# Performance work log

Hardware: AMD Instinct MI355X
Metric: run time of the kernel (lower is better)

## Reference

```python
import jax, jax.numpy as jnp
import numpy as np

N_QUBITS = 16
N_LAYERS = 2
NUM_CLASSES = 10
BATCH = 256

# CNOT as (c_out, t_out, c_in, t_in)
_CNOT = np.zeros((2, 2, 2, 2), dtype=np.complex64)
_CNOT[0, 0, 0, 0] = 1; _CNOT[0, 1, 0, 1] = 1
_CNOT[1, 1, 1, 0] = 1; _CNOT[1, 0, 1, 1] = 1
CNOT = jnp.asarray(_CNOT)


def rot_matrix(phi, theta, omega):
    # PennyLane Rot = RZ(omega) @ RY(theta) @ RZ(phi)
    c, s = jnp.cos(theta / 2), jnp.sin(theta / 2)
    m00 = jnp.exp(-0.5j * (phi + omega)) * c
    m01 = -jnp.exp(0.5j * (phi - omega)) * s
    m10 = jnp.exp(-0.5j * (phi - omega)) * s
    m11 = jnp.exp(0.5j * (phi + omega)) * c
    return jnp.stack([jnp.stack([m00, m01]), jnp.stack([m10, m11])]).astype(jnp.complex64)


def apply_1q(state, U, w, n):
    # state: (B, 2**n); wire 0 = most-significant bit (PennyLane convention)
    B = state.shape[0]
    st = state.reshape(B, 2 ** w, 2, -1)
    st = jnp.einsum('oi,baic->baoc', U, st)
    return st.reshape(B, -1)


def apply_cnot(state, c, t, n):
    B = state.shape[0]
    st = state.reshape((B,) + (2,) * n)
    st = jnp.tensordot(CNOT, st, axes=[[2, 3], [c + 1, t + 1]])  # new c,t axes at front
    st = jnp.moveaxis(st, [0, 1], [c + 1, t + 1])
    return st.reshape(B, -1)


def circuit_expvals(x, q_params, n, n_layers):
    # AmplitudeEmbedding with normalize=True
    norm = jnp.sqrt(jnp.sum(x * x, axis=-1, keepdims=True))
    psi = (x / norm).astype(jnp.complex64)
    for l in range(n_layers):
        for w in range(n):
            U = rot_matrix(q_params[l, w, 0], q_params[l, w, 1], q_params[l, w, 2])
            psi = apply_1q(psi, U, w, n)
        r = (l % (n - 1)) + 1  # default StronglyEntanglingLayers ranges
        for w in range(n):
            psi = apply_cnot(psi, w, (w + r) % n, n)
    probs = psi.real ** 2 + psi.imag ** 2  # (B, 2**n)
    B = probs.shape[0]
    ev = []
    for w in range(n):
        p = probs.reshape(B, 2 ** w, 2, -1)
        ev.append(p[:, :, 0, :].sum(axis=(1, 2)) - p[:, :, 1, :].sum(axis=(1, 2)))
    return jnp.stack(ev, axis=1)  # (B, n)


def setup_inputs() -> dict:
    key = jax.random.key(0)
    k1, k2, k3, k4 = jax.random.split(key, 4)
    x = jax.random.normal(k1, (BATCH, 2 ** N_QUBITS), dtype=jnp.float32)
    q_params = jax.random.normal(k2, (N_LAYERS, N_QUBITS, 3), dtype=jnp.float32)
    lim = 1.0 / np.sqrt(N_QUBITS)
    W = jax.random.uniform(k3, (NUM_CLASSES, N_QUBITS), jnp.float32, -lim, lim)
    b = jax.random.uniform(k4, (NUM_CLASSES,), jnp.float32, -lim, lim)
    return {"x": x, "q_params": q_params, "W": W, "b": b}


def reference(x, q_params, W, b):
    feats = circuit_expvals(x, q_params, N_QUBITS, N_LAYERS)  # (B, n_qubits)
    return feats @ W.T + b
```

## Files before the change

kernel.cpp:

```cpp
#include <hip/hip_runtime.h>


#define BATCH 256
#define NCLS 10

typedef float v2f __attribute__((ext_vector_type(2)));
typedef _Float16 f16x2 __attribute__((ext_vector_type(2)));

struct CircuitMeta { unsigned l1mask[16]; unsigned l1role[16]; unsigned fin[16]; };

__host__ __device__ constexpr CircuitMeta make_meta() {
  CircuitMeta m{};
  unsigned col[16], inv[16];
  for (int w = 0; w < 16; ++w) { col[w] = 1u << (15 - w); inv[w] = 1u << (15 - w); }
  for (int w = 0; w < 16; ++w) { int c = w, t = (w + 1) & 15; col[c] ^= col[t]; inv[t] ^= inv[c]; }
  for (int w = 0; w < 16; ++w) { m.l1mask[w] = col[w]; m.l1role[w] = inv[w]; }
  for (int w = 0; w < 16; ++w) { int c = w, t = (w + 2) & 15; col[c] ^= col[t]; inv[t] ^= inv[c]; }
  for (int w = 0; w < 16; ++w) m.fin[w] = inv[w];
  return m;
}
constexpr CircuitMeta META = make_meta();

__host__ __device__ constexpr unsigned HASH(unsigned i) {
  return i ^ ((i >> 4) & 15u) ^ ((i >> 8) & 15u);
}

__device__ __forceinline__ v2f swp(v2f a) { return __builtin_shufflevector(a, a, 1, 0); }

__device__ __forceinline__ unsigned PK(v2f a) {
  return __builtin_bit_cast(unsigned, __builtin_amdgcn_cvt_pkrtz(a.x, a.y));
}
__device__ __forceinline__ v2f UNPK(unsigned u) {
  f16x2 h = __builtin_bit_cast(f16x2, u);
  return (v2f){(float)h.x, (float)h.y};
}

template<int B0,int B1,int B2,int B3,int B4>
__host__ __device__ constexpr unsigned regval5(int j) {
  return ((unsigned)(j & 1) << B0) | ((unsigned)((j >> 1) & 1) << B1) |
         ((unsigned)((j >> 2) & 1) << B2) | ((unsigned)((j >> 3) & 1) << B3) |
         ((unsigned)((j >> 4) & 1) << B4);
}

template<int B0,int B1,int B2,int B3,int B4, unsigned MG, unsigned RG>
__device__ __forceinline__ void gate5(v2f (&A)[32], const float* __restrict__ g,
                                      int gi, unsigned tp) {
  constexpr unsigned cover = (1u<<B0)|(1u<<B1)|(1u<<B2)|(1u<<B3)|(1u<<B4);
  static_assert((MG & ~cover) == 0u, "gate mask not covered by stage reg bits");
  constexpr unsigned mr = ((MG>>B0)&1u) | (((MG>>B1)&1u)<<1) | (((MG>>B2)&1u)<<2)
                        | (((MG>>B3)&1u)<<3) | (((MG>>B4)&1u)<<4);
  static_assert(mr != 0u, "empty reg mask");
  constexpr unsigned pivot = mr & (0u - mr);

  float u00r = g[gi*8+0], u00i = g[gi*8+1], u01r = g[gi*8+2], u01i = g[gi*8+3];
  float u10r = g[gi*8+4], u10i = g[gi*8+5], u11r = g[gi*8+6], u11i = g[gi*8+7];
  const bool s = (__popc(RG & tp) & 1) != 0;
  float e00r = s ? u11r : u00r, e00i = s ? u11i : u00i;
  float e01r = s ? u10r : u01r, e01i = s ? u10i : u01i;
  float e10r = s ? u01r : u10r, e10i = s ? u01i : u10i;
  float e11r = s ? u00r : u11r, e11i = s ? u00i : u11i;
  v2f a00 = {e00r, e00r}, b00 = {-e00i, e00i};
  v2f a01 = {e01r, e01r}, b01 = {-e01i, e01i};
  v2f a10 = {e10r, e10r}, b10 = {-e10i, e10i};
  v2f a11 = {e11r, e11r}, b11 = {-e11i, e11i};

  #pragma unroll
  for (int j0 = 0; j0 < 32; ++j0) {
    if (j0 & (int)pivot) continue;
    const int j1 = j0 ^ (int)mr;
    const bool podd =
      (__builtin_popcount(RG & regval5<B0,B1,B2,B3,B4>(j0)) & 1) != 0;
    v2f v0 = A[j0], v1 = A[j1];
    v2f v0s = swp(v0), v1s = swp(v1);
    if (!podd) {
      A[j0] = a00*v0 + b00*v0s + a01*v1 + b01*v1s;
      A[j1] = a10*v0 + b10*v0s + a11*v1 + b11*v1s;
    } else {
      A[j0] = a11*v0 + b11*v0s + a10*v1 + b10*v1s;
      A[j1] = a01*v0 + b01*v0s + a00*v1 + b00*v1s;
    }
  }
}

__global__ void prep_gates(const float* __restrict__ qp, float* __restrict__ g) {
  int i = threadIdx.x;
  if (i >= 32) return;
  float phi = qp[i*3+0], th = qp[i*3+1], om = qp[i*3+2];
  float cth = cosf(0.5f*th), sth = sinf(0.5f*th);
  float a = 0.5f*(phi+om), d = 0.5f*(phi-om);
  float ca = cosf(a), sa = sinf(a), cd = cosf(d), sd = sinf(d);
  g[i*8+0] =  ca*cth; g[i*8+1] = -sa*cth;
  g[i*8+2] = -cd*sth; g[i*8+3] = -sd*sth;
  g[i*8+4] =  cd*sth; g[i*8+5] = -sd*sth;
  g[i*8+6] =  ca*cth; g[i*8+7] =  sa*cth;
}

__global__ __launch_bounds__(256, 4) void passA(const float* __restrict__ x,
    unsigned* __restrict__ st, const float* __restrict__ g) {
  __shared__ unsigned L[8192];
  const int t = threadIdx.x;
  const int batch = blockIdx.x >> 3;
  const unsigned f = blockIdx.x & 7;
  const float* xb = x + ((size_t)batch << 16) + ((size_t)f << 13);

  v2f A[32];
  #pragma unroll
  for (int j = 0; j < 32; ++j) A[j] = (v2f){xb[((unsigned)j << 8) | (unsigned)t], 0.f};

  gate5<8,9,10,11,12, 0x1000u,0x1000u>(A, g, 3, 0u);
  gate5<8,9,10,11,12, 0x0800u,0x0800u>(A, g, 4, 0u);
  gate5<8,9,10,11,12, 0x0400u,0x0400u>(A, g, 5, 0u);
  gate5<8,9,10,11,12, 0x0200u,0x0200u>(A, g, 6, 0u);
  gate5<8,9,10,11,12, 0x0100u,0x0100u>(A, g, 7, 0u);

  {
    const unsigned wb = HASH((unsigned)t);
    #pragma unroll
    for (int j = 0; j < 32; ++j) L[wb ^ HASH((unsigned)j << 8)] = PK(A[j]);
    __syncthreads();
    const unsigned rb = HASH((((unsigned)t & 0xF8u) << 5) | ((unsigned)t & 7u));
    #pragma unroll
    for (int j = 0; j < 32; ++j) A[j] = UNPK(L[rb ^ HASH((unsigned)j << 3)]);
  }

  gate5<3,4,5,6,7, 0x0080u,0x0080u>(A, g,  8, 0u);
  gate5<3,4,5,6,7, 0x0040u,0x0040u>(A, g,  9, 0u);
  gate5<3,4,5,6,7, 0x0020u,0x0020u>(A, g, 10, 0u);
  gate5<3,4,5,6,7, 0x0010u,0x0010u>(A, g, 11, 0u);
  gate5<3,4,5,6,7, 0x0008u,0x0008u>(A, g, 12, 0u);

  __syncthreads();
  {
    const unsigned wb = HASH((((unsigned)t & 0xF8u) << 5) | ((unsigned)t & 7u));
    #pragma unroll
    for (int j = 0; j < 32; ++j) L[wb ^ HASH((unsigned)j << 3)] = PK(A[j]);
    __syncthreads();
    const unsigned rb = HASH((unsigned)t << 3);
    #pragma unroll
    for (int j = 0; j < 32; ++j)
      A[j] = UNPK(L[rb ^ HASH(((unsigned)j & 7u) | (((unsigned)j & 24u) << 8))]);
  }

  gate5<0,1,2,11,12, 0x0004u,0x0004u>(A, g, 13, 0u);
  gate5<0,1,2,11,12, 0x0002u,0x0002u>(A, g, 14, 0u);
  gate5<0,1,2,11,12, 0x0001u,0x0001u>(A, g, 15, 0u);

  unsigned* outb = st + ((size_t)batch << 16) + ((size_t)f << 13);
  #pragma unroll
  for (int jh = 0; jh < 4; ++jh) {
    uint4 q0, q1;
    q0.x = PK(A[jh*8+0]); q0.y = PK(A[jh*8+1]); q0.z = PK(A[jh*8+2]); q0.w = PK(A[jh*8+3]);
    q1.x = PK(A[jh*8+4]); q1.y = PK(A[jh*8+5]); q1.z = PK(A[jh*8+6]); q1.w = PK(A[jh*8+7]);
    const unsigned si = ((unsigned)jh << 11) | ((unsigned)t << 3);
    *(uint4*)(outb + si) = q0;
    *(uint4*)(outb + si + 4) = q1;
  }
}

__global__ __launch_bounds__(256, 4) void passB(unsigned* __restrict__ st,
    const float* __restrict__ g) {
  __shared__ unsigned L[8192];
  const int t = threadIdx.x;
  const int batch = blockIdx.x >> 3;
  const unsigned c = blockIdx.x & 7;
  unsigned* stb = st + ((size_t)batch << 16);

  const unsigned lbase = ((unsigned)t & 127u) | (((unsigned)t & 128u) << 3) | (c << 7);
  v2f A[32];
  #pragma unroll
  for (int j = 0; j < 32; ++j) A[j] = UNPK(stb[((unsigned)j << 11) | lbase]);

  const unsigned tp1 = lbase;
  gate5<11,12,13,14,15, 0x8000u,0x8000u>(A, g, 0, tp1);
  gate5<11,12,13,14,15, 0x4000u,0x4000u>(A, g, 1, tp1);
  gate5<11,12,13,14,15, 0x2000u,0x2000u>(A, g, 2, tp1);
  gate5<11,12,13,14,15, META.l1mask[0], META.l1role[0]>(A, g, 16, tp1);
  gate5<11,12,13,14,15, META.l1mask[1], META.l1role[1]>(A, g, 17, tp1);
  gate5<11,12,13,14,15, META.l1mask[2], META.l1role[2]>(A, g, 18, tp1);
  gate5<11,12,13,14,15, META.l1mask[3], META.l1role[3]>(A, g, 19, tp1);

  {
    const unsigned wb = HASH((unsigned)t);
    #pragma unroll
    for (int j = 0; j < 32; ++j) L[wb ^ HASH((unsigned)j << 8)] = PK(A[j]);
    __syncthreads();
    const unsigned rb = HASH((((unsigned)t & 0xF0u) << 5) | (((unsigned)t & 15u) << 1));
    #pragma unroll
    for (int j = 0; j < 32; ++j)
      A[j] = UNPK(L[rb ^ HASH(((unsigned)j & 1u) | (((unsigned)j & 30u) << 4))]);
  }

  const unsigned tp2 = (((unsigned)t & 0xF0u) << 8) | (((unsigned)t & 15u) << 1) | (c << 7);
  gate5<0,5,6,10,11, META.l1mask[4], META.l1role[4]>(A, g, 20, tp2);
  gate5<0,5,6,10,11, META.l1mask[9], META.l1role[9]>(A, g, 25, tp2);

  __syncthreads();
  {
    const unsigned wb = HASH((((unsigned)t & 0xF0u) << 5) | (((unsigned)t & 15u) << 1));
    #pragma unroll
    for (int j = 0; j < 32; ++j)
      L[wb ^ HASH(((unsigned)j & 1u) | (((unsigned)j & 30u) << 4))] = PK(A[j]);
    __syncthreads();
    const unsigned rb = HASH((((unsigned)t & 0xFEu) << 5) | ((unsigned)t & 1u));
    #pragma unroll
    for (int j = 0; j < 32; ++j) A[j] = UNPK(L[rb ^ HASH((unsigned)j << 1)]);
  }

  const unsigned tp3 = (((unsigned)t & 0xFCu) << 8) | (((unsigned)t & 2u) << 5)
                     | ((unsigned)t & 1u) | (c << 7);
  gate5<1,2,3,4,5, META.l1mask[10], META.l1role[10]>(A, g, 26, tp3);
  gate5<1,2,3,4,5, META.l1mask[11], META.l1role[11]>(A, g, 27, tp3);
  gate5<1,2,3,4,5, META.l1mask[12], META.l1role[12]>(A, g, 28, tp3);
  gate5<1,2,3,4,5, META.l1mask[13], META.l1role[13]>(A, g, 29, tp3);

  __syncthreads();
  {
    const unsigned wb = HASH((((unsigned)t & 0xFEu) << 5) | ((unsigned)t & 1u));
    #pragma unroll
    for (int j = 0; j < 32; ++j) L[wb ^ HASH((unsigned)j << 1)] = PK(A[j]);
    __syncthreads();
    const unsigned rb = HASH((unsigned)t << 2);
    #pragma unroll
    for (int j = 0; j < 32; ++j)
      A[j] = UNPK(L[rb ^ HASH(((unsigned)j & 3u) | (((unsigned)j & 28u) << 8))]);
  }

  const unsigned tp4 = (((unsigned)t & 0xE0u) << 5) | (((unsigned)t & 31u) << 2) | (c << 7);
  gate5<0,1,13,14,15, META.l1mask[14], META.l1role[14]>(A, g, 30, tp4);
  gate5<0,1,13,14,15, META.l1mask[15], META.l1role[15]>(A, g, 31, tp4);

  #pragma unroll
  for (int jh = 0; jh < 8; ++jh) {
    uint4 q;
    q.x = PK(A[jh*4+0]); q.y = PK(A[jh*4+1]); q.z = PK(A[jh*4+2]); q.w = PK(A[jh*4+3]);
    *(uint4*)(stb + (tp4 | ((unsigned)jh << 13))) = q;
  }
}

__global__ __launch_bounds__(256, 4) void passC(const unsigned* __restrict__ st,
    const float* __restrict__ g, float* __restrict__ partials) {
  __shared__ float R[4][17];
  const int t = threadIdx.x;
  const int batch = blockIdx.x >> 3;
  const unsigned f = blockIdx.x & 7;
  const unsigned* stb = st + ((size_t)batch << 16);

  const unsigned cbase = (f << 13) | (((unsigned)t & 192u) << 5) | ((unsigned)t & 63u);
  v2f A[32];
  #pragma unroll
  for (int j = 0; j < 32; ++j) A[j] = UNPK(stb[cbase | ((unsigned)j << 6)]);

  gate5<6,7,8,9,10, META.l1mask[5], META.l1role[5]>(A, g, 21, cbase);
  gate5<6,7,8,9,10, META.l1mask[6], META.l1role[6]>(A, g, 22, cbase);
  gate5<6,7,8,9,10, META.l1mask[7], META.l1role[7]>(A, g, 23, cbase);
  gate5<6,7,8,9,10, META.l1mask[8], META.l1role[8]>(A, g, 24, cbase);

  float sv[16], tot = 0.f;
  #pragma unroll
  for (int w = 0; w < 16; ++w) sv[w] = 0.f;
  #pragma unroll
  for (int j = 0; j < 32; ++j) {
    const float pr = A[j].x*A[j].x + A[j].y*A[j].y;
    tot += pr;
    #pragma unroll
    for (int w = 0; w < 16; ++w) {
      const bool neg = (__builtin_popcount(META.fin[w] & ((unsigned)j << 6)) & 1) != 0;
      sv[w] += neg ? -pr : pr;
    }
  }
  #pragma unroll
  for (int w = 0; w < 16; ++w)
    if (__popc(META.fin[w] & cbase) & 1) sv[w] = -sv[w];

  #pragma unroll
  for (int off = 32; off; off >>= 1) {
    tot += __shfl_xor(tot, off, 64);
    #pragma unroll
    for (int w = 0; w < 16; ++w) sv[w] += __shfl_xor(sv[w], off, 64);
  }
  const int wave = t >> 6, lane = t & 63;
  if (lane == 0) {
    #pragma unroll
    for (int w = 0; w < 16; ++w) R[wave][w] = sv[w];
    R[wave][16] = tot;
  }
  __syncthreads();
  if (t < 17) {
    const float s2 = R[0][t] + R[1][t] + R[2][t] + R[3][t];
    partials[(size_t)blockIdx.x * 17 + t] = s2;
  }
}

__global__ __launch_bounds__(64) void head(const float* __restrict__ partials,
    const float* __restrict__ W, const float* __restrict__ bias,
    float* __restrict__ out) {
  const int b = blockIdx.x, tid = threadIdx.x;
  __shared__ float red[17];
  __shared__ float ev[16];
  if (tid < 17) {
    float s = 0.f;
    #pragma unroll
    for (int ch = 0; ch < 8; ++ch) s += partials[(size_t)((b << 3) + ch) * 17 + tid];
    red[tid] = s;
  }
  __syncthreads();
  if (tid < 16) ev[tid] = red[tid] / red[16];
  __syncthreads();
  if (tid < NCLS) {
    float o = bias[tid];
    #pragma unroll
    for (int w = 0; w < 16; ++w) o += ev[w] * W[tid*16 + w];
    out[b*NCLS + tid] = o;
  }
}

extern "C" void kernel_launch(void* const* d_in, const int* in_sizes, int n_in,
                              void* d_out, int out_size, void* d_ws, size_t ws_size,
                              hipStream_t stream) {
  const float* x  = (const float*)d_in[0];
  const float* qp = (const float*)d_in[1];
  const float* W  = (const float*)d_in[2];
  const float* bv = (const float*)d_in[3];
  float* out = (float*)d_out;

  unsigned* st     = (unsigned*)d_ws;
  float*    gates  = (float*)((char*)d_ws + (size_t)BATCH * 65536 * 4);
  float*    parts  = (float*)((char*)gates + 1024);

  prep_gates<<<dim3(1), dim3(64), 0, stream>>>(qp, gates);
  passA<<<dim3(BATCH*8), dim3(256), 0, stream>>>(x, st, gates);
  passB<<<dim3(BATCH*8), dim3(256), 0, stream>>>(st, gates);
  passC<<<dim3(BATCH*8), dim3(256), 0, stream>>>(st, gates, parts);
  head<<<dim3(BATCH), dim3(64), 0, stream>>>(parts, W, bv, out);
}
```

Baseline: 197.8 us.

## Fuse all passes into one per-batch kernel holding full state in LDS/registers

Replaces the three global-memory passes and the head kernel with a single kernel that runs one block of 1024 threads per batch element. Each thread holds 64 packed fp16 amplitudes in registers, and qubit reorderings are done through 128KB of dynamic LDS in two halves. Gates are regrouped into six stages, and the final reduction and linear head are folded into the same kernel. This removes the global state round-trips between passes and two kernel launches. In exchange it raises register pressure, allows only 256 blocks in the grid, and adds several barriers per exchange.

```diff
diff --git a/kernel.cpp b/kernel.cpp
--- a/kernel.cpp
+++ b/kernel.cpp
@@ -11,7 +11,7 @@
 
 __host__ __device__ constexpr CircuitMeta make_meta() {
   CircuitMeta m{};
-  unsigned col[16], inv[16];
+  unsigned col[16] = {}, inv[16] = {};
   for (int w = 0; w < 16; ++w) { col[w] = 1u << (15 - w); inv[w] = 1u << (15 - w); }
   for (int w = 0; w < 16; ++w) { int c = w, t = (w + 1) & 15; col[c] ^= col[t]; inv[t] ^= inv[c]; }
   for (int w = 0; w < 16; ++w) { m.l1mask[w] = col[w]; m.l1role[w] = inv[w]; }
@@ -21,12 +21,33 @@
 }
 constexpr CircuitMeta META = make_meta();
 
-__host__ __device__ constexpr unsigned HASH(unsigned i) {
-  return i ^ ((i >> 4) & 15u) ^ ((i >> 8) & 15u);
-}
+__host__ __device__ constexpr unsigned XH(unsigned q) {
+  return q ^ ((q >> 5) & 31u) ^ ((q >> 10) & 31u);
+}
+template<int H> __host__ __device__ constexpr unsigned QDROP(unsigned i) {
+  return (i & ((1u << H) - 1u)) | ((i >> (H + 1)) << H);
+}
+
+__host__ __device__ constexpr unsigned tg1(unsigned t){ return t << 2; }
+__host__ __device__ constexpr unsigned tg2(unsigned t){ return (t & 63u) | (((t >> 6) & 15u) << 12); }
+__host__ __device__ constexpr unsigned tg3(unsigned t){ return ((t & 31u) << 6) | (((t >> 5) & 15u) << 12) | (((t >> 9) & 1u) << 11); }
+__host__ __device__ constexpr unsigned tg4(unsigned t){ return (t & 31u) | (((t >> 5) & 15u) << 6) | (((t >> 9) & 1u) << 5); }
+__host__ __device__ constexpr unsigned tg5(unsigned t){ return (t & 31u) | (((t >> 5) & 31u) << 11); }
+__host__ __device__ constexpr unsigned tg6(unsigned t){ return ((t & 63u) << 4) | (((t >> 6) & 7u) << 11) | (((t >> 9) & 1u) << 10); }
+
+template<int B0,int B1,int B2,int B3,int B4,int B5>
+__host__ __device__ constexpr unsigned rv6b(unsigned j) {
+  return ((j & 1u) << B0) | (((j >> 1) & 1u) << B1) | (((j >> 2) & 1u) << B2) |
+         (((j >> 3) & 1u) << B3) | (((j >> 4) & 1u) << B4) | (((j >> 5) & 1u) << B5);
+}
+__host__ __device__ constexpr unsigned rv_s1(unsigned j){ return rv6b<0,1,12,13,14,15>(j); }
+__host__ __device__ constexpr unsigned rv_s2(unsigned j){ return rv6b<6,7,8,9,10,11>(j); }
+__host__ __device__ constexpr unsigned rv_s3(unsigned j){ return rv6b<0,1,2,3,4,5>(j); }
+__host__ __device__ constexpr unsigned rv_s4(unsigned j){ return rv6b<11,12,13,14,15,10>(j); }
+__host__ __device__ constexpr unsigned rv_s5(unsigned j){ return rv6b<5,6,7,8,9,10>(j); }
+__host__ __device__ constexpr unsigned rv_s6(unsigned j){ return rv6b<0,1,2,3,14,15>(j); }
 
 __device__ __forceinline__ v2f swp(v2f a) { return __builtin_shufflevector(a, a, 1, 0); }
-
 __device__ __forceinline__ unsigned PK(v2f a) {
   return __builtin_bit_cast(unsigned, __builtin_amdgcn_cvt_pkrtz(a.x, a.y));
 }
@@ -35,20 +56,13 @@
   return (v2f){(float)h.x, (float)h.y};
 }
 
-template<int B0,int B1,int B2,int B3,int B4>
-__host__ __device__ constexpr unsigned regval5(int j) {
-  return ((unsigned)(j & 1) << B0) | ((unsigned)((j >> 1) & 1) << B1) |
-         ((unsigned)((j >> 2) & 1) << B2) | ((unsigned)((j >> 3) & 1) << B3) |
-         ((unsigned)((j >> 4) & 1) << B4);
-}
-
-template<int B0,int B1,int B2,int B3,int B4, unsigned MG, unsigned RG>
-__device__ __forceinline__ void gate5(v2f (&A)[32], const float* __restrict__ g,
+template<int B0,int B1,int B2,int B3,int B4,int B5, unsigned MG, unsigned RG>
+__device__ __forceinline__ void gate6(unsigned (&A)[64], const float* __restrict__ g,
                                       int gi, unsigned tp) {
-  constexpr unsigned cover = (1u<<B0)|(1u<<B1)|(1u<<B2)|(1u<<B3)|(1u<<B4);
+  constexpr unsigned cover = (1u<<B0)|(1u<<B1)|(1u<<B2)|(1u<<B3)|(1u<<B4)|(1u<<B5);
   static_assert((MG & ~cover) == 0u, "gate mask not covered by stage reg bits");
   constexpr unsigned mr = ((MG>>B0)&1u) | (((MG>>B1)&1u)<<1) | (((MG>>B2)&1u)<<2)
-                        | (((MG>>B3)&1u)<<3) | (((MG>>B4)&1u)<<4);
+                        | (((MG>>B3)&1u)<<3) | (((MG>>B4)&1u)<<4) | (((MG>>B5)&1u)<<5);
   static_assert(mr != 0u, "empty reg mask");
   constexpr unsigned pivot = mr & (0u - mr);
 
@@ -65,19 +79,19 @@
   v2f a11 = {e11r, e11r}, b11 = {-e11i, e11i};
 
   #pragma unroll
-  for (int j0 = 0; j0 < 32; ++j0) {
+  for (int j0 = 0; j0 < 64; ++j0) {
     if (j0 & (int)pivot) continue;
     const int j1 = j0 ^ (int)mr;
     const bool podd =
-      (__builtin_popcount(RG & regval5<B0,B1,B2,B3,B4>(j0)) & 1) != 0;
-    v2f v0 = A[j0], v1 = A[j1];
+      (__builtin_popcount(RG & rv6b<B0,B1,B2,B3,B4,B5>((unsigned)j0)) & 1) != 0;
+    v2f v0 = UNPK(A[j0]), v1 = UNPK(A[j1]);
     v2f v0s = swp(v0), v1s = swp(v1);
     if (!podd) {
-      A[j0] = a00*v0 + b00*v0s + a01*v1 + b01*v1s;
-      A[j1] = a10*v0 + b10*v0s + a11*v1 + b11*v1s;
+      A[j0] = PK(a00*v0 + b00*v0s + a01*v1 + b01*v1s);
+      A[j1] = PK(a10*v0 + b10*v0s + a11*v1 + b11*v1s);
     } else {
-      A[j0] = a11*v0 + b11*v0s + a10*v1 + b10*v1s;
-      A[j1] = a01*v0 + b01*v0s + a00*v1 + b00*v1s;
+      A[j0] = PK(a11*v0 + b11*v0s + a10*v1 + b10*v1s);
+      A[j1] = PK(a01*v0 + b01*v0s + a00*v1 + b00*v1s);
     }
   }
 }
@@ -95,182 +109,143 @@
   g[i*8+6] =  ca*cth; g[i*8+7] =  sa*cth;
 }
 
-__global__ __launch_bounds__(256, 4) void passA(const float* __restrict__ x,
-    unsigned* __restrict__ st, const float* __restrict__ g) {
-  __shared__ unsigned L[8192];
-  const int t = threadIdx.x;
-  const int batch = blockIdx.x >> 3;
-  const unsigned f = blockIdx.x & 7;
-  const float* xb = x + ((size_t)batch << 16) + ((size_t)f << 13);
-
-  v2f A[32];
-  #pragma unroll
-  for (int j = 0; j < 32; ++j) A[j] = (v2f){xb[((unsigned)j << 8) | (unsigned)t], 0.f};
-
-  gate5<8,9,10,11,12, 0x1000u,0x1000u>(A, g, 3, 0u);
-  gate5<8,9,10,11,12, 0x0800u,0x0800u>(A, g, 4, 0u);
-  gate5<8,9,10,11,12, 0x0400u,0x0400u>(A, g, 5, 0u);
-  gate5<8,9,10,11,12, 0x0200u,0x0200u>(A, g, 6, 0u);
-  gate5<8,9,10,11,12, 0x0100u,0x0100u>(A, g, 7, 0u);
-
-  {
-    const unsigned wb = HASH((unsigned)t);
-    #pragma unroll
-    for (int j = 0; j < 32; ++j) L[wb ^ HASH((unsigned)j << 8)] = PK(A[j]);
-    __syncthreads();
-    const unsigned rb = HASH((((unsigned)t & 0xF8u) << 5) | ((unsigned)t & 7u));
-    #pragma unroll
-    for (int j = 0; j < 32; ++j) A[j] = UNPK(L[rb ^ HASH((unsigned)j << 3)]);
-  }
-
-  gate5<3,4,5,6,7, 0x0080u,0x0080u>(A, g,  8, 0u);
-  gate5<3,4,5,6,7, 0x0040u,0x0040u>(A, g,  9, 0u);
-  gate5<3,4,5,6,7, 0x0020u,0x0020u>(A, g, 10, 0u);
-  gate5<3,4,5,6,7, 0x0010u,0x0010u>(A, g, 11, 0u);
-  gate5<3,4,5,6,7, 0x0008u,0x0008u>(A, g, 12, 0u);
-
-  __syncthreads();
-  {
-    const unsigned wb = HASH((((unsigned)t & 0xF8u) << 5) | ((unsigned)t & 7u));
-    #pragma unroll
-    for (int j = 0; j < 32; ++j) L[wb ^ HASH((unsigned)j << 3)] = PK(A[j]);
-    __syncthreads();
-    const unsigned rb = HASH((unsigned)t << 3);
-    #pragma unroll
-    for (int j = 0; j < 32; ++j)
-      A[j] = UNPK(L[rb ^ HASH(((unsigned)j & 7u) | (((unsigned)j & 24u) << 8))]);
-  }
-
-  gate5<0,1,2,11,12, 0x0004u,0x0004u>(A, g, 13, 0u);
-  gate5<0,1,2,11,12, 0x0002u,0x0002u>(A, g, 14, 0u);
-  gate5<0,1,2,11,12, 0x0001u,0x0001u>(A, g, 15, 0u);
-
-  unsigned* outb = st + ((size_t)batch << 16) + ((size_t)f << 13);
-  #pragma unroll
-  for (int jh = 0; jh < 4; ++jh) {
-    uint4 q0, q1;
-    q0.x = PK(A[jh*8+0]); q0.y = PK(A[jh*8+1]); q0.z = PK(A[jh*8+2]); q0.w = PK(A[jh*8+3]);
-    q1.x = PK(A[jh*8+4]); q1.y = PK(A[jh*8+5]); q1.z = PK(A[jh*8+6]); q1.w = PK(A[jh*8+7]);
-    const unsigned si = ((unsigned)jh << 11) | ((unsigned)t << 3);
-    *(uint4*)(outb + si) = q0;
-    *(uint4*)(outb + si + 4) = q1;
-  }
-}
-
-__global__ __launch_bounds__(256, 4) void passB(unsigned* __restrict__ st,
-    const float* __restrict__ g) {
-  __shared__ unsigned L[8192];
-  const int t = threadIdx.x;
-  const int batch = blockIdx.x >> 3;
-  const unsigned c = blockIdx.x & 7;
-  unsigned* stb = st + ((size_t)batch << 16);
-
-  const unsigned lbase = ((unsigned)t & 127u) | (((unsigned)t & 128u) << 3) | (c << 7);
-  v2f A[32];
-  #pragma unroll
-  for (int j = 0; j < 32; ++j) A[j] = UNPK(stb[((unsigned)j << 11) | lbase]);
-
-  const unsigned tp1 = lbase;
-  gate5<11,12,13,14,15, 0x8000u,0x8000u>(A, g, 0, tp1);
-  gate5<11,12,13,14,15, 0x4000u,0x4000u>(A, g, 1, tp1);
-  gate5<11,12,13,14,15, 0x2000u,0x2000u>(A, g, 2, tp1);
-  gate5<11,12,13,14,15, META.l1mask[0], META.l1role[0]>(A, g, 16, tp1);
-  gate5<11,12,13,14,15, META.l1mask[1], META.l1role[1]>(A, g, 17, tp1);
-  gate5<11,12,13,14,15, META.l1mask[2], META.l1role[2]>(A, g, 18, tp1);
-  gate5<11,12,13,14,15, META.l1mask[3], META.l1role[3]>(A, g, 19, tp1);
-
-  {
-    const unsigned wb = HASH((unsigned)t);
-    #pragma unroll
-    for (int j = 0; j < 32; ++j) L[wb ^ HASH((unsigned)j << 8)] = PK(A[j]);
-    __syncthreads();
-    const unsigned rb = HASH((((unsigned)t & 0xF0u) << 5) | (((unsigned)t & 15u) << 1));
-    #pragma unroll
-    for (int j = 0; j < 32; ++j)
-      A[j] = UNPK(L[rb ^ HASH(((unsigned)j & 1u) | (((unsigned)j & 30u) << 4))]);
-  }
-
-  const unsigned tp2 = (((unsigned)t & 0xF0u) << 8) | (((unsigned)t & 15u) << 1) | (c << 7);
-  gate5<0,5,6,10,11, META.l1mask[4], META.l1role[4]>(A, g, 20, tp2);
-  gate5<0,5,6,10,11, META.l1mask[9], META.l1role[9]>(A, g, 25, tp2);
-
-  __syncthreads();
-  {
-    const unsigned wb = HASH((((unsigned)t & 0xF0u) << 5) | (((unsigned)t & 15u) << 1));
-    #pragma unroll
-    for (int j = 0; j < 32; ++j)
-      L[wb ^ HASH(((unsigned)j & 1u) | (((unsigned)j & 30u) << 4))] = PK(A[j]);
-    __syncthreads();
-    const unsigned rb = HASH((((unsigned)t & 0xFEu) << 5) | ((unsigned)t & 1u));
-    #pragma unroll
-    for (int j = 0; j < 32; ++j) A[j] = UNPK(L[rb ^ HASH((unsigned)j << 1)]);
-  }
-
-  const unsigned tp3 = (((unsigned)t & 0xFCu) << 8) | (((unsigned)t & 2u) << 5)
-                     | ((unsigned)t & 1u) | (c << 7);
-  gate5<1,2,3,4,5, META.l1mask[10], META.l1role[10]>(A, g, 26, tp3);
-  gate5<1,2,3,4,5, META.l1mask[11], META.l1role[11]>(A, g, 27, tp3);
-  gate5<1,2,3,4,5, META.l1mask[12], META.l1role[12]>(A, g, 28, tp3);
-  gate5<1,2,3,4,5, META.l1mask[13], META.l1role[13]>(A, g, 29, tp3);
-
-  __syncthreads();
-  {
-    const unsigned wb = HASH((((unsigned)t & 0xFEu) << 5) | ((unsigned)t & 1u));
-    #pragma unroll
-    for (int j = 0; j < 32; ++j) L[wb ^ HASH((unsigned)j << 1)] = PK(A[j]);
-    __syncthreads();
-    const unsigned rb = HASH((unsigned)t << 2);
-    #pragma unroll
-    for (int j = 0; j < 32; ++j)
-      A[j] = UNPK(L[rb ^ HASH(((unsigned)j & 3u) | (((unsigned)j & 28u) << 8))]);
-  }
-
-  const unsigned tp4 = (((unsigned)t & 0xE0u) << 5) | (((unsigned)t & 31u) << 2) | (c << 7);
-  gate5<0,1,13,14,15, META.l1mask[14], META.l1role[14]>(A, g, 30, tp4);
-  gate5<0,1,13,14,15, META.l1mask[15], META.l1role[15]>(A, g, 31, tp4);
-
-  #pragma unroll
-  for (int jh = 0; jh < 8; ++jh) {
-    uint4 q;
-    q.x = PK(A[jh*4+0]); q.y = PK(A[jh*4+1]); q.z = PK(A[jh*4+2]); q.w = PK(A[jh*4+3]);
-    *(uint4*)(stb + (tp4 | ((unsigned)jh << 13))) = q;
-  }
-}
-
-__global__ __launch_bounds__(256, 4) void passC(const unsigned* __restrict__ st,
-    const float* __restrict__ g, float* __restrict__ partials) {
-  __shared__ float R[4][17];
-  const int t = threadIdx.x;
-  const int batch = blockIdx.x >> 3;
-  const unsigned f = blockIdx.x & 7;
-  const unsigned* stb = st + ((size_t)batch << 16);
-
-  const unsigned cbase = (f << 13) | (((unsigned)t & 192u) << 5) | ((unsigned)t & 63u);
-  v2f A[32];
-  #pragma unroll
-  for (int j = 0; j < 32; ++j) A[j] = UNPK(stb[cbase | ((unsigned)j << 6)]);
-
-  gate5<6,7,8,9,10, META.l1mask[5], META.l1role[5]>(A, g, 21, cbase);
-  gate5<6,7,8,9,10, META.l1mask[6], META.l1role[6]>(A, g, 22, cbase);
-  gate5<6,7,8,9,10, META.l1mask[7], META.l1role[7]>(A, g, 23, cbase);
-  gate5<6,7,8,9,10, META.l1mask[8], META.l1role[8]>(A, g, 24, cbase);
+#define EXCH_TMP(HH, TGIN, RVIN, TGOUT, RVOUT)                                   \
+  {                                                                              \
+    const unsigned qbw = XH(QDROP<HH>(TGIN(t)));                                 \
+    const unsigned qbr = XH(QDROP<HH>(TGOUT(t)));                                \
+    const bool rlow = ((t >> 9) & 1u) == 0u;                                     \
+    _Pragma("unroll")                                                            \
+    for (int j = 0; j < 32; ++j) L[qbw ^ XH(QDROP<HH>(RVIN((unsigned)j)))] = A[j]; \
+    __syncthreads();                                                             \
+    if (rlow) {                                                                  \
+      _Pragma("unroll")                                                          \
+      for (int j = 0; j < 32; ++j) A[j] = L[qbr ^ XH(QDROP<HH>(RVOUT((unsigned)j)))]; \
+      _Pragma("unroll")                                                          \
+      for (int j = 0; j < 32; ++j) T[j] = L[qbr ^ XH(QDROP<HH>(RVOUT((unsigned)j + 32u)))]; \
+    }                                                                            \
+    __syncthreads();                                                             \
+    _Pragma("unroll")                                                            \
+    for (int j = 32; j < 64; ++j) L[qbw ^ XH(QDROP<HH>(RVIN((unsigned)j)))] = A[j]; \
+    __syncthreads();                                                             \
+    if (!rlow) {                                                                 \
+      _Pragma("unroll")                                                          \
+      for (int j = 0; j < 64; ++j) A[j] = L[qbr ^ XH(QDROP<HH>(RVOUT((unsigned)j)))]; \
+    } else {                                                                     \
+      _Pragma("unroll")                                                          \
+      for (int j = 0; j < 32; ++j) A[32 + j] = T[j];                             \
+    }                                                                            \
+    __syncthreads();                                                             \
+  }
+
+#define EXCH_SHR(HH, TGIN, RVIN, TGOUT, RVOUT)                                   \
+  {                                                                              \
+    const unsigned qbw = XH(QDROP<HH>(TGIN(t)));                                 \
+    const unsigned qbr = XH(QDROP<HH>(TGOUT(t)));                                \
+    _Pragma("unroll")                                                            \
+    for (int j = 0; j < 32; ++j) L[qbw ^ XH(QDROP<HH>(RVIN((unsigned)j)))] = A[j]; \
+    __syncthreads();                                                             \
+    _Pragma("unroll")                                                            \
+    for (int j = 0; j < 32; ++j) A[j] = L[qbr ^ XH(QDROP<HH>(RVOUT((unsigned)j)))]; \
+    __syncthreads();                                                             \
+    _Pragma("unroll")                                                            \
+    for (int j = 32; j < 64; ++j) L[qbw ^ XH(QDROP<HH>(RVIN((unsigned)j)))] = A[j]; \
+    __syncthreads();                                                             \
+    _Pragma("unroll")                                                            \
+    for (int j = 32; j < 64; ++j) A[j] = L[qbr ^ XH(QDROP<HH>(RVOUT((unsigned)j)))]; \
+    __syncthreads();                                                             \
+  }
+
+__global__ __launch_bounds__(1024, 4) void qsim(
+    const float* __restrict__ x, const float* __restrict__ g,
+    const float* __restrict__ W, const float* __restrict__ bias,
+    float* __restrict__ out)
+{
+  extern __shared__ unsigned L[];
+  const unsigned t = threadIdx.x;
+  unsigned A[64];
+  unsigned T[32];
+
+  const float4* xb = (const float4*)(x + ((size_t)blockIdx.x << 16));
+  #pragma unroll
+  for (int jh = 0; jh < 16; ++jh) {
+    float4 v = xb[((unsigned)jh << 10) | t];
+    A[jh*4+0] = PK((v2f){v.x, 0.f});
+    A[jh*4+1] = PK((v2f){v.y, 0.f});
+    A[jh*4+2] = PK((v2f){v.z, 0.f});
+    A[jh*4+3] = PK((v2f){v.w, 0.f});
+  }
+
+  const unsigned tp1 = tg1(t);
+  gate6<0,1,12,13,14,15, 0x8000u,0x8000u>(A, g,  0, tp1);
+  gate6<0,1,12,13,14,15, 0x4000u,0x4000u>(A, g,  1, tp1);
+  gate6<0,1,12,13,14,15, 0x2000u,0x2000u>(A, g,  2, tp1);
+  gate6<0,1,12,13,14,15, 0x1000u,0x1000u>(A, g,  3, tp1);
+  gate6<0,1,12,13,14,15, 0x0002u,0x0002u>(A, g, 14, tp1);
+  gate6<0,1,12,13,14,15, 0x0001u,0x0001u>(A, g, 15, tp1);
+
+  EXCH_TMP(15, tg1, rv_s1, tg2, rv_s2)
+
+  const unsigned tp2 = tg2(t);
+  gate6<6,7,8,9,10,11, 0x0800u,0x0800u>(A, g, 4, tp2);
+  gate6<6,7,8,9,10,11, 0x0400u,0x0400u>(A, g, 5, tp2);
+  gate6<6,7,8,9,10,11, 0x0200u,0x0200u>(A, g, 6, tp2);
+  gate6<6,7,8,9,10,11, 0x0100u,0x0100u>(A, g, 7, tp2);
+  gate6<6,7,8,9,10,11, 0x0080u,0x0080u>(A, g, 8, tp2);
+  gate6<6,7,8,9,10,11, 0x0040u,0x0040u>(A, g, 9, tp2);
+
+  EXCH_TMP(11, tg2, rv_s2, tg3, rv_s3)
+
+  const unsigned tp3 = tg3(t);
+  gate6<0,1,2,3,4,5, 0x0020u,0x0020u>(A, g, 10, tp3);
+  gate6<0,1,2,3,4,5, 0x0010u,0x0010u>(A, g, 11, tp3);
+  gate6<0,1,2,3,4,5, 0x0008u,0x0008u>(A, g, 12, tp3);
+  gate6<0,1,2,3,4,5, 0x0004u,0x0004u>(A, g, 13, tp3);
+  gate6<0,1,2,3,4,5, META.l1mask[10], META.l1role[10]>(A, g, 26, tp3);
+  gate6<0,1,2,3,4,5, META.l1mask[11], META.l1role[11]>(A, g, 27, tp3);
+  gate6<0,1,2,3,4,5, META.l1mask[12], META.l1role[12]>(A, g, 28, tp3);
+  gate6<0,1,2,3,4,5, META.l1mask[13], META.l1role[13]>(A, g, 29, tp3);
+  gate6<0,1,2,3,4,5, META.l1mask[14], META.l1role[14]>(A, g, 30, tp3);
+
+  EXCH_TMP(5, tg3, rv_s3, tg4, rv_s4)
+
+  const unsigned tp4 = tg4(t);
+  gate6<11,12,13,14,15,10, META.l1mask[0], META.l1role[0]>(A, g, 16, tp4);
+  gate6<11,12,13,14,15,10, META.l1mask[1], META.l1role[1]>(A, g, 17, tp4);
+  gate6<11,12,13,14,15,10, META.l1mask[2], META.l1role[2]>(A, g, 18, tp4);
+  gate6<11,12,13,14,15,10, META.l1mask[3], META.l1role[3]>(A, g, 19, tp4);
+  gate6<11,12,13,14,15,10, META.l1mask[4], META.l1role[4]>(A, g, 20, tp4);
+
+  EXCH_SHR(10, tg4, rv_s4, tg5, rv_s5)
+
+  const unsigned tp5 = tg5(t);
+  gate6<5,6,7,8,9,10, META.l1mask[5], META.l1role[5]>(A, g, 21, tp5);
+  gate6<5,6,7,8,9,10, META.l1mask[6], META.l1role[6]>(A, g, 22, tp5);
+  gate6<5,6,7,8,9,10, META.l1mask[7], META.l1role[7]>(A, g, 23, tp5);
+  gate6<5,6,7,8,9,10, META.l1mask[8], META.l1role[8]>(A, g, 24, tp5);
+  gate6<5,6,7,8,9,10, META.l1mask[9], META.l1role[9]>(A, g, 25, tp5);
+
+  EXCH_TMP(10, tg5, rv_s5, tg6, rv_s6)
+
+  const unsigned tp6 = tg6(t);
+  gate6<0,1,2,3,14,15, META.l1mask[15], META.l1role[15]>(A, g, 31, tp6);
 
   float sv[16], tot = 0.f;
   #pragma unroll
   for (int w = 0; w < 16; ++w) sv[w] = 0.f;
   #pragma unroll
-  for (int j = 0; j < 32; ++j) {
-    const float pr = A[j].x*A[j].x + A[j].y*A[j].y;
+  for (int j = 0; j < 64; ++j) {
+    v2f a = UNPK(A[j]);
+    const float pr = a.x*a.x + a.y*a.y;
     tot += pr;
     #pragma unroll
     for (int w = 0; w < 16; ++w) {
-      const bool neg = (__builtin_popcount(META.fin[w] & ((unsigned)j << 6)) & 1) != 0;
+      const bool neg = (__builtin_popcount(META.fin[w] & rv_s6((unsigned)j)) & 1) != 0;
       sv[w] += neg ? -pr : pr;
     }
   }
   #pragma unroll
   for (int w = 0; w < 16; ++w)
-    if (__popc(META.fin[w] & cbase) & 1) sv[w] = -sv[w];
+    if (__popc(META.fin[w] & tp6) & 1) sv[w] = -sv[w];
 
   #pragma unroll
   for (int off = 32; off; off >>= 1) {
@@ -278,58 +253,47 @@
     #pragma unroll
     for (int w = 0; w < 16; ++w) sv[w] += __shfl_xor(sv[w], off, 64);
   }
-  const int wave = t >> 6, lane = t & 63;
+  float* RF = (float*)L;
+  const unsigned wave = t >> 6, lane = t & 63u;
   if (lane == 0) {
     #pragma unroll
-    for (int w = 0; w < 16; ++w) R[wave][w] = sv[w];
-    R[wave][16] = tot;
+    for (int w = 0; w < 16; ++w) RF[wave*17 + w] = sv[w];
+    RF[wave*17 + 16] = tot;
   }
   __syncthreads();
   if (t < 17) {
-    const float s2 = R[0][t] + R[1][t] + R[2][t] + R[3][t];
-    partials[(size_t)blockIdx.x * 17 + t] = s2;
-  }
-}
-
-__global__ __launch_bounds__(64) void head(const float* __restrict__ partials,
-    const float* __restrict__ W, const float* __restrict__ bias,
-    float* __restrict__ out) {
-  const int b = blockIdx.x, tid = threadIdx.x;
-  __shared__ float red[17];
-  __shared__ float ev[16];
-  if (tid < 17) {
-    float s = 0.f;
-    #pragma unroll
-    for (int ch = 0; ch < 8; ++ch) s += partials[(size_t)((b << 3) + ch) * 17 + tid];
-    red[tid] = s;
+    float s2 = 0.f;
+    #pragma unroll
+    for (int wv = 0; wv < 16; ++wv) s2 += RF[wv*17 + t];
+    RF[272 + t] = s2;
   }
   __syncthreads();
-  if (tid < 16) ev[tid] = red[tid] / red[16];
-  __syncthreads();
-  if (tid < NCLS) {
-    float o = bias[tid];
-    #pragma unroll
-    for (int w = 0; w < 16; ++w) o += ev[w] * W[tid*16 + w];
-    out[b*NCLS + tid] = o;
+  if (t < NCLS) {
+    const float tt = RF[272 + 16];
+    float o = bias[t];
+    #pragma unroll
+    for (int w = 0; w < 16; ++w) o += (RF[272 + w] / tt) * W[t*16 + w];
+    out[blockIdx.x * NCLS + t] = o;
   }
 }
 
 extern "C" void kernel_launch(void* const* d_in, const int* in_sizes, int n_in,
                               void* d_out, int out_size, void* d_ws, size_t ws_size,
                               hipStream_t stream) {
+  (void)in_sizes; (void)n_in; (void)out_size; (void)ws_size;
   const float* x  = (const float*)d_in[0];
   const float* qp = (const float*)d_in[1];
   const float* W  = (const float*)d_in[2];
   const float* bv = (const float*)d_in[3];
   float* out = (float*)d_out;
 
-  unsigned* st     = (unsigned*)d_ws;
-  float*    gates  = (float*)((char*)d_ws + (size_t)BATCH * 65536 * 4);
-  float*    parts  = (float*)((char*)gates + 1024);
+  float* gates = (float*)d_ws;
+
+  static_cast<void>(hipFuncSetAttribute(
+      reinterpret_cast<const void*>(&qsim),
+      hipFuncAttributeMaxDynamicSharedMemorySize, 131072));
 
   prep_gates<<<dim3(1), dim3(64), 0, stream>>>(qp, gates);
-  passA<<<dim3(BATCH*8), dim3(256), 0, stream>>>(x, st, gates);
-  passB<<<dim3(BATCH*8), dim3(256), 0, stream>>>(st, gates);
-  passC<<<dim3(BATCH*8), dim3(256), 0, stream>>>(st, gates, parts);
-  head<<<dim3(BATCH), dim3(64), 0, stream>>>(parts, W, bv, out);
-}
+  qsim<<<dim3(BATCH), dim3(1024), 131072, stream>>>(x, gates, (const float*)W,
+                                                    (const float*)bv, out);
+}
```

Measured after the change: 307.2 us. +55.3%, slower.
